# Kernel optimization log

Measured on AMD Instinct MI355X. Metric: run time of the kernel, lower is better.

## Reference

```python
import jax, jax.numpy as jnp
import numpy as np

B, LN, LT, D, DIN, H = 8, 64, 256, 1024, 2048, 4
LN_EPS = 1e-5
F16_EPS = float(np.finfo(np.float16).eps)


def setup_inputs() -> dict:
    key = jax.random.key(0)
    ks = jax.random.split(key, 16)
    n = lambda k, sh: jax.random.normal(k, sh, dtype=jnp.float32)
    s = 0.02
    z = lambda sh: jnp.zeros(sh, jnp.float32)
    return {
        "text_embeds": n(ks[0], (B, LT, D)),
        "node_embeds": n(ks[1], (B, LN, D)),
        "Wq": n(ks[2], (D, H * D)) * s, "bq": z((H * D,)),
        "Wk": n(ks[3], (D, H * D)) * s, "bk": z((H * D,)),
        "Wv": n(ks[4], (D, H * D)) * s, "bv": z((H * D,)),
        "Wo": n(ks[5], (H * D, D)) * s, "bo": z((D,)),
        "ln_g": jnp.ones((D,), jnp.float32), "ln_b": z((D,)),
        "aqW": n(ks[6], (D, D)) * s, "aqb": z((D,)),
        "akW": n(ks[7], (D, D)) * s, "akb": z((D,)),
        "att_v": n(ks[8], (D,)) * (1.0 / np.sqrt(D)),
        "att_b": z((D,)),
        "dp1W": n(ks[9], (D, DIN // 2)) * s, "dp1b": z((DIN // 2,)),
        "dp2W": n(ks[10], (DIN // 2, DIN)) * s, "dp2b": z((DIN,)),
        "gnn_mask": jax.random.randint(ks[11], (B, LN), 0, 2),
        "lm_mask": jax.random.randint(ks[12], (B, LT), 0, 2),
    }


def _forward(text_embeds, node_embeds, Wq, bq, Wk, bk, Wv, bv, Wo, bo, ln_g, ln_b,
             aqW, aqb, akW, akb, att_v, att_b, dp1W, dp1b, dp2W, dp2b,
             gnn_mask, lm_mask):
    x = node_embeds  # (B, LN, D)

    # ---- selfAttention_prompt: each of 4 heads has full width D ----
    def heads(w, b):
        return (x @ w + b).reshape(B, LN, H, D).transpose(0, 2, 1, 3)  # (B,H,LN,D)

    Q, K, V = heads(Wq, bq), heads(Wk, bk), heads(Wv, bv)
    A = jnp.einsum('bhqd,bhkd->bhqk', Q, K) / jnp.sqrt(jnp.float32(D))
    A = jnp.where(gnn_mask[:, None, None, :] == 0, -jnp.inf, A)
    alpha = jax.nn.softmax(A, axis=-1)
    out = jnp.einsum('bhqk,bhkd->bhqd', alpha, V)
    out = out.transpose(0, 2, 1, 3).reshape(B, LN, H * D)
    out = out @ Wo + bo + x
    # LayerNorm (torch default eps=1e-5)
    mu = out.mean(-1, keepdims=True)
    var = ((out - mu) ** 2).mean(-1, keepdims=True)
    H2 = (out - mu) / jnp.sqrt(var + LN_EPS) * ln_g + ln_b  # (B, LN, D)

    # ---- AdditiveAttention (Bahdanau): value_proj is unused in the original ----
    q = H2 @ aqW + aqb            # (B, LN, D)
    k = text_embeds @ akW + akb   # (B, LT, D)
    e = jnp.einsum('bqkd,d->bqk',
                   jnp.tanh(q[:, :, None, :] + k[:, None, :, :] + att_b), att_v)
    e = jnp.where(lm_mask[:, None, :] == 0, -jnp.inf, e)
    w = jax.nn.softmax(e, axis=-1)            # (B, LN, LT)
    H3 = jnp.einsum('bqk,bkd->bqd', w, text_embeds)  # context with raw V

    # ---- filter_Pool: masked mean over nodes ----
    m = gnn_mask.astype(H3.dtype)[:, :, None]
    cnt = jnp.clip(m.sum(1), F16_EPS, None)   # (B, 1)
    H4 = (H3 * m).sum(1) / cnt                # (B, D)

    # ---- domain projector (exact GELU like torch) ----
    Z = jax.nn.gelu(H4 @ dp1W + dp1b, approximate=False) @ dp2W + dp2b
    return Z  # (B, DIN)


def reference(text_embeds, node_embeds, Wq, bq, Wk, bk, Wv, bv, Wo, bo, ln_g, ln_b,
              aqW, aqb, akW, akb, att_v, att_b, dp1W, dp1b, dp2W, dp2b,
              gnn_mask, lm_mask):
    return _forward(text_embeds, node_embeds, Wq, bq, Wk, bk, Wv, bv, Wo, bo,
                    ln_g, ln_b, aqW, aqb, akW, akb, att_v, att_b,
                    dp1W, dp1b, dp2W, dp2b, gnn_mask, lm_mask)
```

## Files before the change

### kernel.cpp

```cpp
#include <hip/hip_runtime.h>
#include <hip/hip_bf16.h>
#include <math.h>

#define NB 8
#define LNN 64
#define LTN 256
#define DD 1024
#define NH 4
#define HDD 4096
#define DINN 2048
#define DHN 1024

#define C_TANH 2.8853900817779268f

typedef __bf16 bf16x8 __attribute__((ext_vector_type(8)));
typedef float f32x4 __attribute__((ext_vector_type(4)));

__device__ __forceinline__ ushort f2b(float f) {
  unsigned int u = __builtin_bit_cast(unsigned int, f);
  u = (u + 0x7FFFu + ((u >> 16) & 1u)) >> 16;
  return (ushort)u;
}

__global__ __launch_bounds__(256) void prep(const float* __restrict__ node,
                                            ushort* __restrict__ node_bf,
                                            const float* __restrict__ text,
                                            ushort* __restrict__ text_bf,
                                            const float* __restrict__ Wq,
                                            const float* __restrict__ Wk,
                                            const float* __restrict__ Wv,
                                            const float* __restrict__ Wo,
                                            const float* __restrict__ aqW,
                                            const float* __restrict__ akW,
                                            ushort* __restrict__ TwtQKV,
                                            ushort* __restrict__ TwtWo,
                                            ushort* __restrict__ TwtAQ) {
  int bid = blockIdx.x;
  int t = threadIdx.x;
  if (bid < 1280) {
    const float* in;
    ushort* out;
    int i;
    if (bid < 256) { in = node; out = node_bf; i = (bid * 256 + t) * 8; }
    else { in = text; out = text_bf; i = ((bid - 256) * 256 + t) * 8; }
    float4 a = *(const float4*)(in + i);
    float4 b = *(const float4*)(in + i + 4);
    ushort4 o0 = {f2b(a.x), f2b(a.y), f2b(a.z), f2b(a.w)};
    ushort4 o1 = {f2b(b.x), f2b(b.y), f2b(b.z), f2b(b.w)};
    *(ushort4*)(out + i) = o0;
    *(ushort4*)(out + i + 4) = o1;
    return;
  }
  bid -= 1280;
  const float* W;
  ushort* dst0;
  int K, N, tt;
  if (bid < 3072) {
    int z = bid >> 10;
    tt = bid & 1023;
    W = (z == 0) ? Wq : ((z == 1) ? Wk : Wv);
    dst0 = TwtQKV + (size_t)z * DD * HDD;
    K = DD; N = HDD;
  } else if (bid < 4096) {
    tt = bid - 3072; W = Wo; dst0 = TwtWo; K = HDD; N = DD;
  } else if (bid < 4352) {
    tt = bid - 4096; W = aqW; dst0 = TwtAQ; K = DD; N = DD;
  } else {
    tt = bid - 4352; W = akW; dst0 = TwtAQ + (size_t)DD * DD; K = DD; N = DD;
  }
  int ntn = N >> 6;
  int n0 = (tt % ntn) << 6, k0 = (tt / ntn) << 6;
  __shared__ float tf[64][65];
  int r = t >> 2, c4 = (t & 3) * 16;
  const float* src = W + (size_t)(k0 + r) * N + n0 + c4;
  float4 v0 = *(const float4*)(src);
  float4 v1 = *(const float4*)(src + 4);
  float4 v2 = *(const float4*)(src + 8);
  float4 v3 = *(const float4*)(src + 12);
  *(float4*)&tf[r][c4] = v0;
  *(float4*)&tf[r][c4 + 4] = v1;
  *(float4*)&tf[r][c4 + 8] = v2;
  *(float4*)&tf[r][c4 + 12] = v3;
  __syncthreads();
  int nl = t >> 2, kc = (t & 3) * 16;
  ushort tmp[16];
#pragma unroll
  for (int j = 0; j < 16; ++j) tmp[j] = f2b(tf[kc + j][nl]);
  ushort* dst = dst0 + (size_t)(n0 + nl) * K + k0 + kc;
  *(uint4*)(dst) = *(uint4*)&tmp[0];
  *(uint4*)(dst + 8) = *(uint4*)&tmp[8];
}

__global__ __launch_bounds__(256) void gemm_qkv3(const ushort* __restrict__ A,
                                                 const ushort* __restrict__ BtB,
                                                 const float* __restrict__ b0,
                                                 const float* __restrict__ b1,
                                                 const float* __restrict__ b2,
                                                 ushort* __restrict__ o0,
                                                 ushort* __restrict__ o1,
                                                 ushort* __restrict__ o2,
                                                 int M, int N, int K) {
  int z = blockIdx.z;
  const ushort* Bt = BtB + (size_t)z * N * K;
  const float* bias = (z == 0) ? b0 : ((z == 1) ? b1 : b2);
  ushort* Cout = (z == 0) ? o0 : ((z == 1) ? o1 : o2);
  __shared__ ushort Als[64 * 64];
  __shared__ ushort Bls[128 * 64];
  int tid = threadIdx.x;
  int m0 = blockIdx.y << 6, n0 = blockIdx.x << 7;
  int srow = tid >> 3, su = tid & 7;
  int sx = (su ^ (srow & 7)) * 8;
  const ushort* ga = A + (size_t)(m0 + srow) * K + su * 8;
  const ushort* gb = Bt + (size_t)(n0 + srow) * K + su * 8;
  int wa0 = srow * 64 + sx, wa1 = (srow + 32) * 64 + sx;
  int wb2 = (srow + 64) * 64 + sx, wb3 = (srow + 96) * 64 + sx;
  const size_t rs32 = (size_t)32 * K;
  int lane = tid & 63, w = tid >> 6;
  int wm = w >> 1, wn = w & 1;
  int r = lane & 15, kg = lane >> 4;
  f32x4 acc[2][4] = {};
  uint4 pa0 = *(const uint4*)(ga);
  uint4 pa1 = *(const uint4*)(ga + rs32);
  uint4 pb0 = *(const uint4*)(gb);
  uint4 pb1 = *(const uint4*)(gb + rs32);
  uint4 pb2 = *(const uint4*)(gb + 2 * rs32);
  uint4 pb3 = *(const uint4*)(gb + 3 * rs32);
  for (int k0 = 0; k0 < K; k0 += 64) {
    __syncthreads();
    *(uint4*)&Als[wa0] = pa0; *(uint4*)&Als[wa1] = pa1;
    *(uint4*)&Bls[wa0] = pb0; *(uint4*)&Bls[wa1] = pb1;
    *(uint4*)&Bls[wb2] = pb2; *(uint4*)&Bls[wb3] = pb3;
    __syncthreads();
    int kn = k0 + 64;
    if (kn < K) {
      pa0 = *(const uint4*)(ga + kn);
      pa1 = *(const uint4*)(ga + rs32 + kn);
      pb0 = *(const uint4*)(gb + kn);
      pb1 = *(const uint4*)(gb + rs32 + kn);
      pb2 = *(const uint4*)(gb + 2 * rs32 + kn);
      pb3 = *(const uint4*)(gb + 3 * rs32 + kn);
    }
#pragma unroll
    for (int h = 0; h < 2; ++h) {
      int sa = ((h * 4 + kg) ^ (r & 7)) * 8;
      bf16x8 af[2], bfr[4];
#pragma unroll
      for (int m = 0; m < 2; ++m)
        af[m] = *(const bf16x8*)&Als[(wm * 32 + m * 16 + r) * 64 + sa];
#pragma unroll
      for (int n = 0; n < 4; ++n)
        bfr[n] = *(const bf16x8*)&Bls[(wn * 64 + n * 16 + r) * 64 + sa];
#pragma unroll
      for (int m = 0; m < 2; ++m)
#pragma unroll
        for (int n = 0; n < 4; ++n)
          acc[m][n] = __builtin_amdgcn_mfma_f32_16x16x32_bf16(af[m], bfr[n], acc[m][n], 0, 0, 0);
    }
  }
#pragma unroll
  for (int m = 0; m < 2; ++m)
#pragma unroll
    for (int n = 0; n < 4; ++n) {
      f32x4 a = acc[m][n];
#pragma unroll
      for (int v = 0; v < 4; ++v) {
        int row = m0 + wm * 32 + m * 16 + kg * 4 + v;
        int col = n0 + wn * 64 + n * 16 + r;
        Cout[(size_t)row * N + col] = f2b(a[v] + bias[col]);
      }
    }
}

__global__ __launch_bounds__(256) void gemm_wo_split(const ushort* __restrict__ A,
                                                     const ushort* __restrict__ Bt,
                                                     float* __restrict__ P,
                                                     int M, int N, int K) {
  __shared__ ushort Als[64 * 64];
  __shared__ ushort Bls[128 * 64];
  int tid = threadIdx.x;
  int m0 = blockIdx.y << 6, n0 = blockIdx.x << 7;
  int Ks = K >> 2, kbase = blockIdx.z * Ks;
  int srow = tid >> 3, su = tid & 7;
  int sx = (su ^ (srow & 7)) * 8;
  const ushort* ga = A + (size_t)(m0 + srow) * K + kbase + su * 8;
  const ushort* gb = Bt + (size_t)(n0 + srow) * K + kbase + su * 8;
  int wa0 = srow * 64 + sx, wa1 = (srow + 32) * 64 + sx;
  int wb2 = (srow + 64) * 64 + sx, wb3 = (srow + 96) * 64 + sx;
  const size_t rs32 = (size_t)32 * K;
  int lane = tid & 63, w = tid >> 6;
  int wm = w >> 1, wn = w & 1;
  int r = lane & 15, kg = lane >> 4;
  f32x4 acc[2][4] = {};
  uint4 pa0 = *(const uint4*)(ga);
  uint4 pa1 = *(const uint4*)(ga + rs32);
  uint4 pb0 = *(const uint4*)(gb);
  uint4 pb1 = *(const uint4*)(gb + rs32);
  uint4 pb2 = *(const uint4*)(gb + 2 * rs32);
  uint4 pb3 = *(const uint4*)(gb + 3 * rs32);
  for (int k0 = 0; k0 < Ks; k0 += 64) {
    __syncthreads();
    *(uint4*)&Als[wa0] = pa0; *(uint4*)&Als[wa1] = pa1;
    *(uint4*)&Bls[wa0] = pb0; *(uint4*)&Bls[wa1] = pb1;
    *(uint4*)&Bls[wb2] = pb2; *(uint4*)&Bls[wb3] = pb3;
    __syncthreads();
    int kn = k0 + 64;
    if (kn < Ks) {
      pa0 = *(const uint4*)(ga + kn);
      pa1 = *(const uint4*)(ga + rs32 + kn);
      pb0 = *(const uint4*)(gb + kn);
      pb1 = *(const uint4*)(gb + rs32 + kn);
      pb2 = *(const uint4*)(gb + 2 * rs32 + kn);
      pb3 = *(const uint4*)(gb + 3 * rs32 + kn);
    }
#pragma unroll
    for (int h = 0; h < 2; ++h) {
      int sa = ((h * 4 + kg) ^ (r & 7)) * 8;
      bf16x8 af[2], bfr[4];
#pragma unroll
      for (int m = 0; m < 2; ++m)
        af[m] = *(const bf16x8*)&Als[(wm * 32 + m * 16 + r) * 64 + sa];
#pragma unroll
      for (int n = 0; n < 4; ++n)
        bfr[n] = *(const bf16x8*)&Bls[(wn * 64 + n * 16 + r) * 64 + sa];
#pragma unroll
      for (int m = 0; m < 2; ++m)
#pragma unroll
        for (int n = 0; n < 4; ++n)
          acc[m][n] = __builtin_amdgcn_mfma_f32_16x16x32_bf16(af[m], bfr[n], acc[m][n], 0, 0, 0);
    }
  }
#pragma unroll
  for (int m = 0; m < 2; ++m)
#pragma unroll
    for (int n = 0; n < 4; ++n) {
      f32x4 a = acc[m][n];
#pragma unroll
      for (int v = 0; v < 4; ++v) {
        int row = m0 + wm * 32 + m * 16 + kg * 4 + v;
        int col = n0 + wn * 64 + n * 16 + r;
        P[((size_t)blockIdx.z * M + row) * N + col] = a[v];
      }
    }
}

__global__ __launch_bounds__(256) void gemm_aqak(const ushort* __restrict__ H2,
                                                 const ushort* __restrict__ Tbf,
                                                 const ushort* __restrict__ TwtAQ,
                                                 const float* __restrict__ aqb,
                                                 const float* __restrict__ akb,
                                                 const float* __restrict__ attb,
                                                 float* __restrict__ QBu,
                                                 float* __restrict__ KAB,
                                                 int N, int K) {
  __shared__ ushort Als[64 * 64];
  __shared__ ushort Bls[128 * 64];
  int tid = threadIdx.x;
  int gm0 = blockIdx.y << 6, n0 = blockIdx.x << 7;
  const ushort* Abase;
  const ushort* Bt;
  const float* bias;
  const float* bias2;
  float* Obase;
  if (gm0 < 512) {
    Abase = H2 + (size_t)gm0 * K;
    Bt = TwtAQ;
    bias = aqb; bias2 = nullptr;
    Obase = QBu + (size_t)gm0 * N;
  } else {
    Abase = Tbf + (size_t)(gm0 - 512) * K;
    Bt = TwtAQ + (size_t)N * K;
    bias = akb; bias2 = attb;
    Obase = KAB + (size_t)(gm0 - 512) * N;
  }
  int srow = tid >> 3, su = tid & 7;
  int sx = (su ^ (srow & 7)) * 8;
  const ushort* ga = Abase + (size_t)srow * K + su * 8;
  const ushort* gb = Bt + (size_t)(n0 + srow) * K + su * 8;
  int wa0 = srow * 64 + sx, wa1 = (srow + 32) * 64 + sx;
  int wb2 = (srow + 64) * 64 + sx, wb3 = (srow + 96) * 64 + sx;
  const size_t rs32 = (size_t)32 * K;
  int lane = tid & 63, w = tid >> 6;
  int wm = w >> 1, wn = w & 1;
  int r = lane & 15, kg = lane >> 4;
  f32x4 acc[2][4] = {};
  uint4 pa0 = *(const uint4*)(ga);
  uint4 pa1 = *(const uint4*)(ga + rs32);
  uint4 pb0 = *(const uint4*)(gb);
  uint4 pb1 = *(const uint4*)(gb + rs32);
  uint4 pb2 = *(const uint4*)(gb + 2 * rs32);
  uint4 pb3 = *(const uint4*)(gb + 3 * rs32);
  for (int k0 = 0; k0 < K; k0 += 64) {
    __syncthreads();
    *(uint4*)&Als[wa0] = pa0; *(uint4*)&Als[wa1] = pa1;
    *(uint4*)&Bls[wa0] = pb0; *(uint4*)&Bls[wa1] = pb1;
    *(uint4*)&Bls[wb2] = pb2; *(uint4*)&Bls[wb3] = pb3;
    __syncthreads();
    int kn = k0 + 64;
    if (kn < K) {
      pa0 = *(const uint4*)(ga + kn);
      pa1 = *(const uint4*)(ga + rs32 + kn);
      pb0 = *(const uint4*)(gb + kn);
      pb1 = *(const uint4*)(gb + rs32 + kn);
      pb2 = *(const uint4*)(gb + 2 * rs32 + kn);
      pb3 = *(const uint4*)(gb + 3 * rs32 + kn);
    }
#pragma unroll
    for (int h = 0; h < 2; ++h) {
      int sa = ((h * 4 + kg) ^ (r & 7)) * 8;
      bf16x8 af[2], bfr[4];
#pragma unroll
      for (int m = 0; m < 2; ++m)
        af[m] = *(const bf16x8*)&Als[(wm * 32 + m * 16 + r) * 64 + sa];
#pragma unroll
      for (int n = 0; n < 4; ++n)
        bfr[n] = *(const bf16x8*)&Bls[(wn * 64 + n * 16 + r) * 64 + sa];
#pragma unroll
      for (int m = 0; m < 2; ++m)
#pragma unroll
        for (int n = 0; n < 4; ++n)
          acc[m][n] = __builtin_amdgcn_mfma_f32_16x16x32_bf16(af[m], bfr[n], acc[m][n], 0, 0, 0);
    }
  }
#pragma unroll
  for (int m = 0; m < 2; ++m)
#pragma unroll
    for (int n = 0; n < 4; ++n) {
      f32x4 a = acc[m][n];
#pragma unroll
      for (int v = 0; v < 4; ++v) {
        int lrow = wm * 32 + m * 16 + kg * 4 + v;
        int col = n0 + wn * 64 + n * 16 + r;
        float x = a[v] + bias[col];
        if (bias2) x += bias2[col];
        Obase[(size_t)lrow * N + col] = x * C_TANH;
      }
    }
}

__global__ __launch_bounds__(256) void wo_ln(const float* __restrict__ P,
                                             const float* __restrict__ bo,
                                             const float* __restrict__ node,
                                             const float* __restrict__ g,
                                             const float* __restrict__ be,
                                             ushort* __restrict__ Y) {
  int row = blockIdx.x, tid = threadIdx.x;
  int c = tid * 4;
  const size_t MN = (size_t)512 * 1024;
  size_t o = (size_t)row * DD + c;
  float4 v0 = *(const float4*)(P + o);
  float4 v1 = *(const float4*)(P + MN + o);
  float4 v2 = *(const float4*)(P + 2 * MN + o);
  float4 v3 = *(const float4*)(P + 3 * MN + o);
  float4 rv = *(const float4*)(node + o);
  float4 bv = *(const float4*)(bo + c);
  float4 v;
  v.x = v0.x + v1.x + v2.x + v3.x + rv.x + bv.x;
  v.y = v0.y + v1.y + v2.y + v3.y + rv.y + bv.y;
  v.z = v0.z + v1.z + v2.z + v3.z + rv.z + bv.z;
  v.w = v0.w + v1.w + v2.w + v3.w + rv.w + bv.w;
  float s = v.x + v.y + v.z + v.w;
  float ss = v.x * v.x + v.y * v.y + v.z * v.z + v.w * v.w;
  for (int o2 = 32; o2; o2 >>= 1) {
    s += __shfl_xor(s, o2, 64);
    ss += __shfl_xor(ss, o2, 64);
  }
  __shared__ float rb_[8];
  int lane = tid & 63, w = tid >> 6;
  if (lane == 0) { rb_[w] = s; rb_[4 + w] = ss; }
  __syncthreads();
  s = rb_[0] + rb_[1] + rb_[2] + rb_[3];
  ss = rb_[4] + rb_[5] + rb_[6] + rb_[7];
  float mu = s * (1.f / 1024.f);
  float var = ss * (1.f / 1024.f) - mu * mu;
  float rstd = rsqrtf(var + 1e-5f);
  ushort4 o4;
  o4.x = f2b((v.x - mu) * rstd * g[c + 0] + be[c + 0]);
  o4.y = f2b((v.y - mu) * rstd * g[c + 1] + be[c + 1]);
  o4.z = f2b((v.z - mu) * rstd * g[c + 2] + be[c + 2]);
  o4.w = f2b((v.w - mu) * rstd * g[c + 3] + be[c + 3]);
  *(ushort4*)(Y + (size_t)row * DD + c) = o4;
}

__global__ __launch_bounds__(256) void attn_qk(const ushort* __restrict__ Qb,
                                               const ushort* __restrict__ Kb,
                                               float* __restrict__ Sp) {
  int bh = blockIdx.x, ks = blockIdx.y;
  int b = bh >> 2;
  size_t base = ((size_t)b * LNN) * HDD + (size_t)(bh & 3) * DD + ks * 128;
  __shared__ ushort Als[64 * 64];
  __shared__ ushort Bls[64 * 64];
  int tid = threadIdx.x;
  int srow = tid >> 2, su0 = (tid & 3) * 2;
  const ushort* ga = Qb + base + (size_t)srow * HDD + su0 * 8;
  const ushort* gb = Kb + base + (size_t)srow * HDD + su0 * 8;
  int wa0 = srow * 64 + ((su0) ^ (srow & 7)) * 8;
  int wa1 = srow * 64 + ((su0 + 1) ^ (srow & 7)) * 8;
  int lane = tid & 63, w = tid >> 6;
  int wm = w >> 1, wn = w & 1;
  int r = lane & 15, kg = lane >> 4;
  f32x4 acc[2][2] = {};
  uint4 pa0 = *(const uint4*)(ga);
  uint4 pa1 = *(const uint4*)(ga + 8);
  uint4 pb0 = *(const uint4*)(gb);
  uint4 pb1 = *(const uint4*)(gb + 8);
  for (int k0 = 0; k0 < 128; k0 += 64) {
    __syncthreads();
    *(uint4*)&Als[wa0] = pa0; *(uint4*)&Als[wa1] = pa1;
    *(uint4*)&Bls[wa0] = pb0; *(uint4*)&Bls[wa1] = pb1;
    __syncthreads();
    if (k0 == 0) {
      pa0 = *(const uint4*)(ga + 64);
      pa1 = *(const uint4*)(ga + 64 + 8);
      pb0 = *(const uint4*)(gb + 64);
      pb1 = *(const uint4*)(gb + 64 + 8);
    }
#pragma unroll
    for (int h = 0; h < 2; ++h) {
      int sa = ((h * 4 + kg) ^ (r & 7)) * 8;
      bf16x8 af[2], bfr[2];
#pragma unroll
      for (int m = 0; m < 2; ++m)
        af[m] = *(const bf16x8*)&Als[(wm * 32 + m * 16 + r) * 64 + sa];
#pragma unroll
      for (int n = 0; n < 2; ++n)
        bfr[n] = *(const bf16x8*)&Bls[(wn * 32 + n * 16 + r) * 64 + sa];
#pragma unroll
      for (int m = 0; m < 2; ++m)
#pragma unroll
        for (int n = 0; n < 2; ++n)
          acc[m][n] = __builtin_amdgcn_mfma_f32_16x16x32_bf16(af[m], bfr[n], acc[m][n], 0, 0, 0);
    }
  }
  float* out = Sp + ((size_t)ks * 32 + bh) * 4096;
#pragma unroll
  for (int m = 0; m < 2; ++m)
#pragma unroll
    for (int n = 0; n < 2; ++n) {
      f32x4 a = acc[m][n];
#pragma unroll
      for (int v = 0; v < 4; ++v) {
        int row = wm * 32 + m * 16 + kg * 4 + v;
        int col = wn * 32 + n * 16 + r;
        out[row * 64 + col] = a[v];
      }
    }
}

__global__ __launch_bounds__(256) void attn_pv(const float* __restrict__ Sp,
                                               const ushort* __restrict__ Vb,
                                               const int* __restrict__ gmask,
                                               ushort* __restrict__ AO) {
  int bid = blockIdx.x;
  int bh = bid >> 3, dt = bid & 7;
  int b = bh >> 2;
  int d0 = dt * 128;
  size_t base = ((size_t)b * LNN) * HDD + (size_t)(bh & 3) * DD;
  __shared__ float S[64][68];
  __shared__ ushort Pls[64 * 72];
  __shared__ ushort Vt[128 * 72];
  int tid = threadIdx.x;
  int lane = tid & 63, w = tid >> 6;
  {
    int fbase = tid * 16;
    float a[16];
#pragma unroll
    for (int i = 0; i < 16; i += 4) {
      float4 v = *(const float4*)(Sp + (size_t)bh * 4096 + fbase + i);
      a[i] = v.x; a[i + 1] = v.y; a[i + 2] = v.z; a[i + 3] = v.w;
    }
#pragma unroll
    for (int ks = 1; ks < 8; ++ks) {
      const float* p = Sp + ((size_t)ks * 32 + bh) * 4096 + fbase;
#pragma unroll
      for (int i = 0; i < 16; i += 4) {
        float4 v = *(const float4*)(p + i);
        a[i] += v.x; a[i + 1] += v.y; a[i + 2] += v.z; a[i + 3] += v.w;
      }
    }
    int q = fbase >> 6, k = fbase & 63;
#pragma unroll
    for (int i = 0; i < 16; ++i) S[q][k + i] = a[i];
  }
  {
    int kq = lane, dq = w * 32;
    const ushort* src = Vb + base + (size_t)kq * HDD + d0 + dq;
    uint4 v0 = *(const uint4*)src;
    uint4 v1 = *(const uint4*)(src + 8);
    uint4 v2 = *(const uint4*)(src + 16);
    uint4 v3 = *(const uint4*)(src + 24);
    ushort tmp[32];
    *(uint4*)&tmp[0] = v0; *(uint4*)&tmp[8] = v1;
    *(uint4*)&tmp[16] = v2; *(uint4*)&tmp[24] = v3;
#pragma unroll
    for (int j = 0; j < 32; ++j) Vt[(dq + j) * 72 + kq] = tmp[j];
  }
  __syncthreads();
  bool valid = gmask[b * LNN + lane] != 0;
  for (int i = 0; i < 16; ++i) {
    int q = w * 16 + i;
    float v = valid ? S[q][lane] * 0.03125f : -__builtin_inff();
    float mx = v;
    for (int o = 32; o; o >>= 1) mx = fmaxf(mx, __shfl_xor(mx, o, 64));
    float e = valid ? __expf(v - mx) : 0.f;
    float s = e;
    for (int o = 32; o; o >>= 1) s += __shfl_xor(s, o, 64);
    Pls[q * 72 + lane] = f2b(__fdividef(e, s));
  }
  __syncthreads();
  int wm = w >> 1, wn = w & 1;
  int r = lane & 15, kg = lane >> 4;
  f32x4 acc[2][4] = {};
#pragma unroll
  for (int h = 0; h < 2; ++h) {
    int ko = h * 32 + kg * 8;
    bf16x8 af[2], bfr[4];
#pragma unroll
    for (int m = 0; m < 2; ++m)
      af[m] = *(const bf16x8*)&Pls[(wm * 32 + m * 16 + r) * 72 + ko];
#pragma unroll
    for (int n = 0; n < 4; ++n)
      bfr[n] = *(const bf16x8*)&Vt[(wn * 64 + n * 16 + r) * 72 + ko];
#pragma unroll
    for (int m = 0; m < 2; ++m)
#pragma unroll
      for (int n = 0; n < 4; ++n)
        acc[m][n] = __builtin_amdgcn_mfma_f32_16x16x32_bf16(af[m], bfr[n], acc[m][n], 0, 0, 0);
  }
#pragma unroll
  for (int m = 0; m < 2; ++m)
#pragma unroll
    for (int n = 0; n < 4; ++n) {
      f32x4 a = acc[m][n];
#pragma unroll
      for (int v = 0; v < 4; ++v) {
        int q = wm * 32 + m * 16 + kg * 4 + v;
        int col = wn * 64 + n * 16 + r;
        AO[base + (size_t)q * HDD + d0 + col] = f2b(a[v]);
      }
    }
}

__global__ __launch_bounds__(256) void addatt_e(const float* __restrict__ QBu,
                                                const float* __restrict__ KAB,
                                                const float* __restrict__ av_,
                                                float* __restrict__ E8) {
  int ds = blockIdx.x, qt = blockIdx.y, b = blockIdx.z;
  int tid = threadIdx.x;
  __shared__ float qs[8][128];
  __shared__ float avs[128];
  __shared__ float red[4];
  int bq0 = b * LNN + qt * 8;
  {
    int qq = tid >> 5, dd = (tid & 31) * 4;
    *(float4*)&qs[qq][dd] = *(const float4*)(QBu + (size_t)(bq0 + qq) * DD + ds * 128 + dd);
  }
  float av = (tid < 128) ? av_[ds * 128 + tid] : 0.f;
  if (tid < 128) avs[tid] = av;
  float s = av;
  for (int o = 32; o; o >>= 1) s += __shfl_xor(s, o, 64);
  int lane = tid & 63, w = tid >> 6;
  if (lane == 0) red[w] = s;
  __syncthreads();
  float sumav = red[0] + red[1] + red[2] + red[3];
  const float* kr = KAB + (size_t)(b * LTN + tid) * DD + ds * 128;
  float ac[8] = {};
#pragma unroll 2
  for (int d = 0; d < 128; d += 4) {
    float4 kv = *(const float4*)(kr + d);
    float4 av4 = *(const float4*)&avs[d];
#pragma unroll
    for (int qq = 0; qq < 8; ++qq) {
      float4 q4 = *(const float4*)&qs[qq][d];
      ac[qq] = fmaf(av4.x, __builtin_amdgcn_rcpf(__builtin_amdgcn_exp2f(q4.x + kv.x) + 1.f), ac[qq]);
      ac[qq] = fmaf(av4.y, __builtin_amdgcn_rcpf(__builtin_amdgcn_exp2f(q4.y + kv.y) + 1.f), ac[qq]);
      ac[qq] = fmaf(av4.z, __builtin_amdgcn_rcpf(__builtin_amdgcn_exp2f(q4.z + kv.z) + 1.f), ac[qq]);
      ac[qq] = fmaf(av4.w, __builtin_amdgcn_rcpf(__builtin_amdgcn_exp2f(q4.w + kv.w) + 1.f), ac[qq]);
    }
  }
  size_t ebase = ((size_t)ds * 512 + bq0) * LTN + tid;
#pragma unroll
  for (int qq = 0; qq < 8; ++qq)
    E8[ebase + (size_t)qq * LTN] = sumav - 2.f * ac[qq];
}

__global__ __launch_bounds__(256) void addatt_sm(const float* __restrict__ E8,
                                                 const int* __restrict__ lmask,
                                                 float* __restrict__ Wv) {
  int bq = blockIdx.x;
  int b = bq >> 6;
  int tid = threadIdx.x;
  __shared__ float rb_[8];
  float e = 0.f;
#pragma unroll
  for (int ks = 0; ks < 8; ++ks)
    e += E8[((size_t)ks * 512 + bq) * LTN + tid];
  bool valid = lmask[b * LTN + tid] != 0;
  float v = valid ? e : -__builtin_inff();
  int lane = tid & 63, w = tid >> 6;
  float m = v;
  for (int o = 32; o; o >>= 1) m = fmaxf(m, __shfl_xor(m, o, 64));
  if (lane == 0) rb_[w] = m;
  __syncthreads();
  m = fmaxf(fmaxf(rb_[0], rb_[1]), fmaxf(rb_[2], rb_[3]));
  float ex = valid ? __expf(v - m) : 0.f;
  float sm = ex;
  for (int o = 32; o; o >>= 1) sm += __shfl_xor(sm, o, 64);
  if (lane == 0) rb_[4 + w] = sm;
  __syncthreads();
  sm = rb_[4] + rb_[5] + rb_[6] + rb_[7];
  Wv[(size_t)bq * LTN + tid] = __fdividef(ex, sm);
}

__global__ __launch_bounds__(256) void addatt_pool(const float* __restrict__ Wv,
                                                   const float* __restrict__ text,
                                                   const int* __restrict__ gmask,
                                                   float* __restrict__ H4) {
  int dt = blockIdx.x, b = blockIdx.y;
  int tid = threadIdx.x;
  __shared__ float cf[LTN];
  float c = 0.f, cnt = 0.f;
#pragma unroll 8
  for (int q = 0; q < LNN; ++q) {
    float m = (gmask[b * LNN + q] != 0) ? 1.f : 0.f;
    cnt += m;
    c = fmaf(m, Wv[(size_t)(b * LNN + q) * LTN + tid], c);
  }
  cf[tid] = c;
  cnt = fmaxf(cnt, 9.765625e-04f);
  __syncthreads();
  int d = dt * 256 + tid;
  const float* tb = text + (size_t)b * LTN * DD + d;
  float acc = 0.f;
#pragma unroll 8
  for (int k = 0; k < LTN; ++k) acc = fmaf(cf[k], tb[(size_t)k * DD], acc);
  H4[b * DD + d] = acc / cnt;
}

__global__ __launch_bounds__(256) void dp_split(const float* __restrict__ X,
                                                const float* __restrict__ W,
                                                float* __restrict__ P,
                                                int K, int N) {
  int jt = blockIdx.x, kt = blockIdx.y;
  int t = threadIdx.x;
  __shared__ float xs[8][32];
  if (t < 64) {
    int b = t >> 3, kk = (t & 7) * 4;
    *(float4*)&xs[b][kk] = *(const float4*)(X + (size_t)b * K + kt * 32 + kk);
  }
  __syncthreads();
  int j = jt * 64 + (t & 63);
  int bg = (t >> 6) * 2;
  const float* wp = W + (size_t)(kt * 32) * N + j;
  float a0 = 0.f, a1 = 0.f;
#pragma unroll
  for (int k = 0; k < 32; ++k) {
    float w = wp[(size_t)k * N];
    a0 = fmaf(xs[bg + 0][k], w, a0);
    a1 = fmaf(xs[bg + 1][k], w, a1);
  }
  P[((size_t)kt * 8 + bg + 0) * N + j] = a0;
  P[((size_t)kt * 8 + bg + 1) * N + j] = a1;
}

template <int GELU>
__global__ __launch_bounds__(256) void dp_reduce(const float* __restrict__ P,
                                                 const float* __restrict__ bias,
                                                 float* __restrict__ O, int N) {
  int b = blockIdx.y;
  int j = blockIdx.x * 256 + threadIdx.x;
  float s = bias[j];
#pragma unroll 8
  for (int kt = 0; kt < 32; ++kt) s += P[((size_t)kt * 8 + b) * N + j];
  if constexpr (GELU) s = 0.5f * s * (1.f + erff(s * 0.70710678118654752440f));
  O[(size_t)b * N + j] = s;
}

extern "C" void kernel_launch(void* const* d_in, const int* in_sizes, int n_in,
                              void* d_out, int out_size, void* d_ws, size_t ws_size,
                              hipStream_t stream) {
  const float* text = (const float*)d_in[0];
  const float* node = (const float*)d_in[1];
  const float* Wq = (const float*)d_in[2];
  const float* bq = (const float*)d_in[3];
  const float* Wk = (const float*)d_in[4];
  const float* bk = (const float*)d_in[5];
  const float* Wv = (const float*)d_in[6];
  const float* bv = (const float*)d_in[7];
  const float* Wo = (const float*)d_in[8];
  const float* bo = (const float*)d_in[9];
  const float* lng = (const float*)d_in[10];
  const float* lnb = (const float*)d_in[11];
  const float* aqW = (const float*)d_in[12];
  const float* aqb = (const float*)d_in[13];
  const float* akW = (const float*)d_in[14];
  const float* akb = (const float*)d_in[15];
  const float* attv = (const float*)d_in[16];
  const float* attb = (const float*)d_in[17];
  const float* dp1W = (const float*)d_in[18];
  const float* dp1b = (const float*)d_in[19];
  const float* dp2W = (const float*)d_in[20];
  const float* dp2b = (const float*)d_in[21];
  const int* gmask = (const int*)d_in[22];
  const int* lmask = (const int*)d_in[23];
  (void)in_sizes; (void)n_in; (void)out_size; (void)ws_size;

  char* base = (char*)d_ws;
#define MB(x) (((size_t)(x)) << 20)
  ushort* TwtQKV = (ushort*)(base);
  ushort* TwtWo = (ushort*)(base + MB(24));
  ushort* TwtAQ = (ushort*)(base + MB(32));
  ushort* node_bf = (ushort*)(base + MB(36));
  ushort* text_bf = (ushort*)(base + MB(37));
  ushort* Qb = (ushort*)(base + MB(41));
  ushort* Kb = (ushort*)(base + MB(45));
  ushort* Vb = (ushort*)(base + MB(49));
  ushort* AO = (ushort*)(base + MB(53));
  float* Sp = (float*)(base + MB(57));
  float* P_Wo = (float*)(base + MB(61));
  ushort* H2 = (ushort*)(base + MB(69));
  float* QBu = (float*)(base + MB(70));
  float* KAB = (float*)(base + MB(72));
  float* E8 = (float*)(base + MB(80));
  float* Wvb = (float*)(base + MB(84));
  float* H4 = (float*)(base + MB(84) + (512 << 10));
  float* G = (float*)(base + MB(84) + (512 << 10) + 32768);
  float* P1 = (float*)(base + MB(85));
  float* P2 = (float*)(base + MB(86));
  float* Z = (float*)d_out;
#undef MB

  const int M1 = NB * LNN;
  dim3 blk(256);

  prep<<<dim3(5888), blk, 0, stream>>>(node, node_bf, text, text_bf,
                                       Wq, Wk, Wv, Wo, aqW, akW,
                                       TwtQKV, TwtWo, TwtAQ);

  gemm_qkv3<<<dim3(HDD / 128, M1 / 64, 3), blk, 0, stream>>>(node_bf, TwtQKV, bq, bk, bv, Qb, Kb, Vb, M1, HDD, DD);

  attn_qk<<<dim3(NB * NH, 8), blk, 0, stream>>>(Qb, Kb, Sp);
  attn_pv<<<dim3(NB * NH * 8), blk, 0, stream>>>(Sp, Vb, gmask, AO);

  gemm_wo_split<<<dim3(DD / 128, M1 / 64, 4), blk, 0, stream>>>(AO, TwtWo, P_Wo, M1, DD, HDD);
  wo_ln<<<dim3(M1), blk, 0, stream>>>(P_Wo, bo, node, lng, lnb, H2);

  gemm_aqak<<<dim3(DD / 128, 40), blk, 0, stream>>>(H2, text_bf, TwtAQ, aqb, akb, attb, QBu, KAB, DD, DD);

  addatt_e<<<dim3(8, 8, NB), blk, 0, stream>>>(QBu, KAB, attv, E8);
  addatt_sm<<<dim3(M1), blk, 0, stream>>>(E8, lmask, Wvb);
  addatt_pool<<<dim3(4, NB), blk, 0, stream>>>(Wvb, text, gmask, H4);

  dp_split<<<dim3(DHN / 64, 32), blk, 0, stream>>>(H4, dp1W, P1, DD, DHN);
  dp_reduce<1><<<dim3(DHN / 256, NB), blk, 0, stream>>>(P1, dp1b, G, DHN);
  dp_split<<<dim3(DINN / 64, 32), blk, 0, stream>>>(G, dp2W, P2, DHN, DINN);
  dp_reduce<0><<<dim3(DINN / 256, NB), blk, 0, stream>>>(P2, dp2b, Z, DINN);
}
```

Before: 162.0 us.

## Use 128x128 GEMM tiles, deepen Wo split-K, fuse GELU reduce into dp2

The three bf16 MFMA GEMMs (QKV, Wo, aq/ak) move from 64x128 to 128x128 tiles, so each warp computes a 64x64 sub-tile (4x4 MFMA accumulators) and more data is reused from LDS per global load. The Wo GEMM split-K factor goes from 4 to 8 to keep enough blocks, and wo_ln now sums 8 partial buffers. The dp1 reduce plus GELU is fused into the dp2 split kernel, dropping one launch and the G buffer round trip, though each block redoes its slice of the reduction. The bigger tiles halve the block count for the QKV and aqak GEMMs and raise register and LDS use per block, which may cut occupancy.

```diff
diff --git a/kernel.cpp b/kernel.cpp
--- a/kernel.cpp
+++ b/kernel.cpp
@@ -91,171 +91,160 @@
   *(uint4*)(dst + 8) = *(uint4*)&tmp[8];
 }
 
-__global__ __launch_bounds__(256) void gemm_qkv3(const ushort* __restrict__ A,
-                                                 const ushort* __restrict__ BtB,
-                                                 const float* __restrict__ b0,
-                                                 const float* __restrict__ b1,
-                                                 const float* __restrict__ b2,
-                                                 ushort* __restrict__ o0,
-                                                 ushort* __restrict__ o1,
-                                                 ushort* __restrict__ o2,
-                                                 int M, int N, int K) {
+
+__global__ __launch_bounds__(256) void gemm128_qkv3(const ushort* __restrict__ A,
+                                                    const ushort* __restrict__ BtB,
+                                                    const float* __restrict__ b0,
+                                                    const float* __restrict__ b1,
+                                                    const float* __restrict__ b2,
+                                                    ushort* __restrict__ o0,
+                                                    ushort* __restrict__ o1,
+                                                    ushort* __restrict__ o2,
+                                                    int M, int N, int K) {
   int z = blockIdx.z;
   const ushort* Bt = BtB + (size_t)z * N * K;
   const float* bias = (z == 0) ? b0 : ((z == 1) ? b1 : b2);
   ushort* Cout = (z == 0) ? o0 : ((z == 1) ? o1 : o2);
-  __shared__ ushort Als[64 * 64];
+  __shared__ ushort Als[128 * 64];
   __shared__ ushort Bls[128 * 64];
   int tid = threadIdx.x;
-  int m0 = blockIdx.y << 6, n0 = blockIdx.x << 7;
-  int srow = tid >> 3, su = tid & 7;
-  int sx = (su ^ (srow & 7)) * 8;
-  const ushort* ga = A + (size_t)(m0 + srow) * K + su * 8;
-  const ushort* gb = Bt + (size_t)(n0 + srow) * K + su * 8;
-  int wa0 = srow * 64 + sx, wa1 = (srow + 32) * 64 + sx;
-  int wb2 = (srow + 64) * 64 + sx, wb3 = (srow + 96) * 64 + sx;
-  const size_t rs32 = (size_t)32 * K;
+  int m0 = blockIdx.y << 7, n0 = blockIdx.x << 7;
+  int srow = tid >> 1, su0 = (tid & 1) * 4;
+  const ushort* ga = A + (size_t)(m0 + srow) * K + su0 * 8;
+  const ushort* gb = Bt + (size_t)(n0 + srow) * K + su0 * 8;
+  int wof[4];
+#pragma unroll
+  for (int j = 0; j < 4; ++j) wof[j] = srow * 64 + ((su0 + j) ^ (srow & 7)) * 8;
   int lane = tid & 63, w = tid >> 6;
   int wm = w >> 1, wn = w & 1;
   int r = lane & 15, kg = lane >> 4;
-  f32x4 acc[2][4] = {};
-  uint4 pa0 = *(const uint4*)(ga);
-  uint4 pa1 = *(const uint4*)(ga + rs32);
-  uint4 pb0 = *(const uint4*)(gb);
-  uint4 pb1 = *(const uint4*)(gb + rs32);
-  uint4 pb2 = *(const uint4*)(gb + 2 * rs32);
-  uint4 pb3 = *(const uint4*)(gb + 3 * rs32);
+  f32x4 acc[4][4] = {};
+  uint4 pa[4], pb[4];
+#pragma unroll
+  for (int j = 0; j < 4; ++j) { pa[j] = *(const uint4*)(ga + j * 8); pb[j] = *(const uint4*)(gb + j * 8); }
   for (int k0 = 0; k0 < K; k0 += 64) {
     __syncthreads();
-    *(uint4*)&Als[wa0] = pa0; *(uint4*)&Als[wa1] = pa1;
-    *(uint4*)&Bls[wa0] = pb0; *(uint4*)&Bls[wa1] = pb1;
-    *(uint4*)&Bls[wb2] = pb2; *(uint4*)&Bls[wb3] = pb3;
+#pragma unroll
+    for (int j = 0; j < 4; ++j) { *(uint4*)&Als[wof[j]] = pa[j]; *(uint4*)&Bls[wof[j]] = pb[j]; }
     __syncthreads();
     int kn = k0 + 64;
     if (kn < K) {
-      pa0 = *(const uint4*)(ga + kn);
-      pa1 = *(const uint4*)(ga + rs32 + kn);
-      pb0 = *(const uint4*)(gb + kn);
-      pb1 = *(const uint4*)(gb + rs32 + kn);
-      pb2 = *(const uint4*)(gb + 2 * rs32 + kn);
-      pb3 = *(const uint4*)(gb + 3 * rs32 + kn);
+#pragma unroll
+      for (int j = 0; j < 4; ++j) {
+        pa[j] = *(const uint4*)(ga + kn + j * 8);
+        pb[j] = *(const uint4*)(gb + kn + j * 8);
+      }
     }
 #pragma unroll
     for (int h = 0; h < 2; ++h) {
       int sa = ((h * 4 + kg) ^ (r & 7)) * 8;
-      bf16x8 af[2], bfr[4];
-#pragma unroll
-      for (int m = 0; m < 2; ++m)
-        af[m] = *(const bf16x8*)&Als[(wm * 32 + m * 16 + r) * 64 + sa];
+      bf16x8 af[4], bfr[4];
+#pragma unroll
+      for (int m = 0; m < 4; ++m)
+        af[m] = *(const bf16x8*)&Als[(wm * 64 + m * 16 + r) * 64 + sa];
 #pragma unroll
       for (int n = 0; n < 4; ++n)
         bfr[n] = *(const bf16x8*)&Bls[(wn * 64 + n * 16 + r) * 64 + sa];
 #pragma unroll
-      for (int m = 0; m < 2; ++m)
+      for (int m = 0; m < 4; ++m)
 #pragma unroll
         for (int n = 0; n < 4; ++n)
           acc[m][n] = __builtin_amdgcn_mfma_f32_16x16x32_bf16(af[m], bfr[n], acc[m][n], 0, 0, 0);
     }
   }
 #pragma unroll
-  for (int m = 0; m < 2; ++m)
+  for (int m = 0; m < 4; ++m)
 #pragma unroll
     for (int n = 0; n < 4; ++n) {
       f32x4 a = acc[m][n];
 #pragma unroll
       for (int v = 0; v < 4; ++v) {
-        int row = m0 + wm * 32 + m * 16 + kg * 4 + v;
+        int row = m0 + wm * 64 + m * 16 + kg * 4 + v;
         int col = n0 + wn * 64 + n * 16 + r;
         Cout[(size_t)row * N + col] = f2b(a[v] + bias[col]);
       }
     }
 }
 
-__global__ __launch_bounds__(256) void gemm_wo_split(const ushort* __restrict__ A,
-                                                     const ushort* __restrict__ Bt,
-                                                     float* __restrict__ P,
-                                                     int M, int N, int K) {
-  __shared__ ushort Als[64 * 64];
+__global__ __launch_bounds__(256) void gemm128_wo(const ushort* __restrict__ A,
+                                                  const ushort* __restrict__ Bt,
+                                                  float* __restrict__ P,
+                                                  int M, int N, int K) {
+  __shared__ ushort Als[128 * 64];
   __shared__ ushort Bls[128 * 64];
   int tid = threadIdx.x;
-  int m0 = blockIdx.y << 6, n0 = blockIdx.x << 7;
-  int Ks = K >> 2, kbase = blockIdx.z * Ks;
-  int srow = tid >> 3, su = tid & 7;
-  int sx = (su ^ (srow & 7)) * 8;
-  const ushort* ga = A + (size_t)(m0 + srow) * K + kbase + su * 8;
-  const ushort* gb = Bt + (size_t)(n0 + srow) * K + kbase + su * 8;
-  int wa0 = srow * 64 + sx, wa1 = (srow + 32) * 64 + sx;
-  int wb2 = (srow + 64) * 64 + sx, wb3 = (srow + 96) * 64 + sx;
-  const size_t rs32 = (size_t)32 * K;
+  int m0 = blockIdx.y << 7, n0 = blockIdx.x << 7;
+  int Ks = K >> 3, kbase = blockIdx.z * Ks;
+  int srow = tid >> 1, su0 = (tid & 1) * 4;
+  const ushort* ga = A + (size_t)(m0 + srow) * K + kbase + su0 * 8;
+  const ushort* gb = Bt + (size_t)(n0 + srow) * K + kbase + su0 * 8;
+  int wof[4];
+#pragma unroll
+  for (int j = 0; j < 4; ++j) wof[j] = srow * 64 + ((su0 + j) ^ (srow & 7)) * 8;
   int lane = tid & 63, w = tid >> 6;
   int wm = w >> 1, wn = w & 1;
   int r = lane & 15, kg = lane >> 4;
-  f32x4 acc[2][4] = {};
-  uint4 pa0 = *(const uint4*)(ga);
-  uint4 pa1 = *(const uint4*)(ga + rs32);
-  uint4 pb0 = *(const uint4*)(gb);
-  uint4 pb1 = *(const uint4*)(gb + rs32);
-  uint4 pb2 = *(const uint4*)(gb + 2 * rs32);
-  uint4 pb3 = *(const uint4*)(gb + 3 * rs32);
+  f32x4 acc[4][4] = {};
+  uint4 pa[4], pb[4];
+#pragma unroll
+  for (int j = 0; j < 4; ++j) { pa[j] = *(const uint4*)(ga + j * 8); pb[j] = *(const uint4*)(gb + j * 8); }
   for (int k0 = 0; k0 < Ks; k0 += 64) {
     __syncthreads();
-    *(uint4*)&Als[wa0] = pa0; *(uint4*)&Als[wa1] = pa1;
-    *(uint4*)&Bls[wa0] = pb0; *(uint4*)&Bls[wa1] = pb1;
-    *(uint4*)&Bls[wb2] = pb2; *(uint4*)&Bls[wb3] = pb3;
+#pragma unroll
+    for (int j = 0; j < 4; ++j) { *(uint4*)&Als[wof[j]] = pa[j]; *(uint4*)&Bls[wof[j]] = pb[j]; }
     __syncthreads();
     int kn = k0 + 64;
     if (kn < Ks) {
-      pa0 = *(const uint4*)(ga + kn);
-      pa1 = *(const uint4*)(ga + rs32 + kn);
-      pb0 = *(const uint4*)(gb + kn);
-      pb1 = *(const uint4*)(gb + rs32 + kn);
-      pb2 = *(const uint4*)(gb + 2 * rs32 + kn);
-      pb3 = *(const uint4*)(gb + 3 * rs32 + kn);
+#pragma unroll
+      for (int j = 0; j < 4; ++j) {
+        pa[j] = *(const uint4*)(ga + kn + j * 8);
+        pb[j] = *(const uint4*)(gb + kn + j * 8);
+      }
     }
 #pragma unroll
     for (int h = 0; h < 2; ++h) {
       int sa = ((h * 4 + kg) ^ (r & 7)) * 8;
-      bf16x8 af[2], bfr[4];
-#pragma unroll
-      for (int m = 0; m < 2; ++m)
-        af[m] = *(const bf16x8*)&Als[(wm * 32 + m * 16 + r) * 64 + sa];
+      bf16x8 af[4], bfr[4];
+#pragma unroll
+      for (int m = 0; m < 4; ++m)
+        af[m] = *(const bf16x8*)&Als[(wm * 64 + m * 16 + r) * 64 + sa];
 #pragma unroll
       for (int n = 0; n < 4; ++n)
         bfr[n] = *(const bf16x8*)&Bls[(wn * 64 + n * 16 + r) * 64 + sa];
 #pragma unroll
-      for (int m = 0; m < 2; ++m)
+      for (int m = 0; m < 4; ++m)
 #pragma unroll
         for (int n = 0; n < 4; ++n)
           acc[m][n] = __builtin_amdgcn_mfma_f32_16x16x32_bf16(af[m], bfr[n], acc[m][n], 0, 0, 0);
     }
   }
 #pragma unroll
-  for (int m = 0; m < 2; ++m)
+  for (int m = 0; m < 4; ++m)
 #pragma unroll
     for (int n = 0; n < 4; ++n) {
       f32x4 a = acc[m][n];
 #pragma unroll
       for (int v = 0; v < 4; ++v) {
-        int row = m0 + wm * 32 + m * 16 + kg * 4 + v;
+        int row = m0 + wm * 64 + m * 16 + kg * 4 + v;
         int col = n0 + wn * 64 + n * 16 + r;
         P[((size_t)blockIdx.z * M + row) * N + col] = a[v];
       }
     }
 }
 
-__global__ __launch_bounds__(256) void gemm_aqak(const ushort* __restrict__ H2,
-                                                 const ushort* __restrict__ Tbf,
-                                                 const ushort* __restrict__ TwtAQ,
-                                                 const float* __restrict__ aqb,
-                                                 const float* __restrict__ akb,
-                                                 const float* __restrict__ attb,
-                                                 float* __restrict__ QBu,
-                                                 float* __restrict__ KAB,
-                                                 int N, int K) {
-  __shared__ ushort Als[64 * 64];
+__global__ __launch_bounds__(256) void gemm128_aqak(const ushort* __restrict__ H2,
+                                                    const ushort* __restrict__ Tbf,
+                                                    const ushort* __restrict__ TwtAQ,
+                                                    const float* __restrict__ aqb,
+                                                    const float* __restrict__ akb,
+                                                    const float* __restrict__ attb,
+                                                    float* __restrict__ QBu,
+                                                    float* __restrict__ KAB,
+                                                    int N, int K) {
+  __shared__ ushort Als[128 * 64];
   __shared__ ushort Bls[128 * 64];
   int tid = threadIdx.x;
-  int gm0 = blockIdx.y << 6, n0 = blockIdx.x << 7;
+  int gm0 = blockIdx.y << 7, n0 = blockIdx.x << 7;
   const ushort* Abase;
   const ushort* Bt;
   const float* bias;
@@ -272,63 +261,57 @@
     bias = akb; bias2 = attb;
     Obase = KAB + (size_t)(gm0 - 512) * N;
   }
-  int srow = tid >> 3, su = tid & 7;
-  int sx = (su ^ (srow & 7)) * 8;
-  const ushort* ga = Abase + (size_t)srow * K + su * 8;
-  const ushort* gb = Bt + (size_t)(n0 + srow) * K + su * 8;
-  int wa0 = srow * 64 + sx, wa1 = (srow + 32) * 64 + sx;
-  int wb2 = (srow + 64) * 64 + sx, wb3 = (srow + 96) * 64 + sx;
-  const size_t rs32 = (size_t)32 * K;
+  int srow = tid >> 1, su0 = (tid & 1) * 4;
+  const ushort* ga = Abase + (size_t)srow * K + su0 * 8;
+  const ushort* gb = Bt + (size_t)(n0 + srow) * K + su0 * 8;
+  int wof[4];
+#pragma unroll
+  for (int j = 0; j < 4; ++j) wof[j] = srow * 64 + ((su0 + j) ^ (srow & 7)) * 8;
   int lane = tid & 63, w = tid >> 6;
   int wm = w >> 1, wn = w & 1;
   int r = lane & 15, kg = lane >> 4;
-  f32x4 acc[2][4] = {};
-  uint4 pa0 = *(const uint4*)(ga);
-  uint4 pa1 = *(const uint4*)(ga + rs32);
-  uint4 pb0 = *(const uint4*)(gb);
-  uint4 pb1 = *(const uint4*)(gb + rs32);
-  uint4 pb2 = *(const uint4*)(gb + 2 * rs32);
-  uint4 pb3 = *(const uint4*)(gb + 3 * rs32);
+  f32x4 acc[4][4] = {};
+  uint4 pa[4], pb[4];
+#pragma unroll
+  for (int j = 0; j < 4; ++j) { pa[j] = *(const uint4*)(ga + j * 8); pb[j] = *(const uint4*)(gb + j * 8); }
   for (int k0 = 0; k0 < K; k0 += 64) {
     __syncthreads();
-    *(uint4*)&Als[wa0] = pa0; *(uint4*)&Als[wa1] = pa1;
-    *(uint4*)&Bls[wa0] = pb0; *(uint4*)&Bls[wa1] = pb1;
-    *(uint4*)&Bls[wb2] = pb2; *(uint4*)&Bls[wb3] = pb3;
+#pragma unroll
+    for (int j = 0; j < 4; ++j) { *(uint4*)&Als[wof[j]] = pa[j]; *(uint4*)&Bls[wof[j]] = pb[j]; }
     __syncthreads();
     int kn = k0 + 64;
     if (kn < K) {
-      pa0 = *(const uint4*)(ga + kn);
-      pa1 = *(const uint4*)(ga + rs32 + kn);
-      pb0 = *(const uint4*)(gb + kn);
-      pb1 = *(const uint4*)(gb + rs32 + kn);
-      pb2 = *(const uint4*)(gb + 2 * rs32 + kn);
-      pb3 = *(const uint4*)(gb + 3 * rs32 + kn);
+#pragma unroll
+      for (int j = 0; j < 4; ++j) {
+        pa[j] = *(const uint4*)(ga + kn + j * 8);
+        pb[j] = *(const uint4*)(gb + kn + j * 8);
+      }
     }
 #pragma unroll
     for (int h = 0; h < 2; ++h) {
       int sa = ((h * 4 + kg) ^ (r & 7)) * 8;
-      bf16x8 af[2], bfr[4];
-#pragma unroll
-      for (int m = 0; m < 2; ++m)
-        af[m] = *(const bf16x8*)&Als[(wm * 32 + m * 16 + r) * 64 + sa];
+      bf16x8 af[4], bfr[4];
+#pragma unroll
+      for (int m = 0; m < 4; ++m)
+        af[m] = *(const bf16x8*)&Als[(wm * 64 + m * 16 + r) * 64 + sa];
 #pragma unroll
       for (int n = 0; n < 4; ++n)
         bfr[n] = *(const bf16x8*)&Bls[(wn * 64 + n * 16 + r) * 64 + sa];
 #pragma unroll
-      for (int m = 0; m < 2; ++m)
+      for (int m = 0; m < 4; ++m)
 #pragma unroll
         for (int n = 0; n < 4; ++n)
           acc[m][n] = __builtin_amdgcn_mfma_f32_16x16x32_bf16(af[m], bfr[n], acc[m][n], 0, 0, 0);
     }
   }
 #pragma unroll
-  for (int m = 0; m < 2; ++m)
+  for (int m = 0; m < 4; ++m)
 #pragma unroll
     for (int n = 0; n < 4; ++n) {
       f32x4 a = acc[m][n];
 #pragma unroll
       for (int v = 0; v < 4; ++v) {
-        int lrow = wm * 32 + m * 16 + kg * 4 + v;
+        int lrow = wm * 64 + m * 16 + kg * 4 + v;
         int col = n0 + wn * 64 + n * 16 + r;
         float x = a[v] + bias[col];
         if (bias2) x += bias2[col];
@@ -347,17 +330,15 @@
   int c = tid * 4;
   const size_t MN = (size_t)512 * 1024;
   size_t o = (size_t)row * DD + c;
-  float4 v0 = *(const float4*)(P + o);
-  float4 v1 = *(const float4*)(P + MN + o);
-  float4 v2 = *(const float4*)(P + 2 * MN + o);
-  float4 v3 = *(const float4*)(P + 3 * MN + o);
   float4 rv = *(const float4*)(node + o);
   float4 bv = *(const float4*)(bo + c);
   float4 v;
-  v.x = v0.x + v1.x + v2.x + v3.x + rv.x + bv.x;
-  v.y = v0.y + v1.y + v2.y + v3.y + rv.y + bv.y;
-  v.z = v0.z + v1.z + v2.z + v3.z + rv.z + bv.z;
-  v.w = v0.w + v1.w + v2.w + v3.w + rv.w + bv.w;
+  v.x = rv.x + bv.x; v.y = rv.y + bv.y; v.z = rv.z + bv.z; v.w = rv.w + bv.w;
+#pragma unroll
+  for (int s8 = 0; s8 < 8; ++s8) {
+    float4 p = *(const float4*)(P + s8 * MN + o);
+    v.x += p.x; v.y += p.y; v.z += p.z; v.w += p.w;
+  }
   float s = v.x + v.y + v.z + v.w;
   float ss = v.x * v.x + v.y * v.y + v.z * v.z + v.w * v.w;
   for (int o2 = 32; o2; o2 >>= 1) {
@@ -662,6 +643,37 @@
   P[((size_t)kt * 8 + bg + 1) * N + j] = a1;
 }
 
+__global__ __launch_bounds__(256) void dp_split2g(const float* __restrict__ P1,
+                                                  const float* __restrict__ b1,
+                                                  const float* __restrict__ W,
+                                                  float* __restrict__ P,
+                                                  int K, int N) {
+  int jt = blockIdx.x, kt = blockIdx.y;
+  int t = threadIdx.x;
+  __shared__ float xs[8][32];
+  {
+    int b = t >> 5, kk = t & 31;
+    int j = kt * 32 + kk;
+    float s = b1[j];
+#pragma unroll 8
+    for (int p = 0; p < 32; ++p) s += P1[((size_t)p * 8 + b) * K + j];
+    xs[b][kk] = 0.5f * s * (1.f + erff(s * 0.70710678118654752440f));
+  }
+  __syncthreads();
+  int j = jt * 64 + (t & 63);
+  int bg = (t >> 6) * 2;
+  const float* wp = W + (size_t)(kt * 32) * N + j;
+  float a0 = 0.f, a1 = 0.f;
+#pragma unroll
+  for (int k = 0; k < 32; ++k) {
+    float w = wp[(size_t)k * N];
+    a0 = fmaf(xs[bg + 0][k], w, a0);
+    a1 = fmaf(xs[bg + 1][k], w, a1);
+  }
+  P[((size_t)kt * 8 + bg + 0) * N + j] = a0;
+  P[((size_t)kt * 8 + bg + 1) * N + j] = a1;
+}
+
 template <int GELU>
 __global__ __launch_bounds__(256) void dp_reduce(const float* __restrict__ P,
                                                  const float* __restrict__ bias,
@@ -717,15 +729,14 @@
   ushort* AO = (ushort*)(base + MB(53));
   float* Sp = (float*)(base + MB(57));
   float* P_Wo = (float*)(base + MB(61));
-  ushort* H2 = (ushort*)(base + MB(69));
-  float* QBu = (float*)(base + MB(70));
-  float* KAB = (float*)(base + MB(72));
-  float* E8 = (float*)(base + MB(80));
-  float* Wvb = (float*)(base + MB(84));
-  float* H4 = (float*)(base + MB(84) + (512 << 10));
-  float* G = (float*)(base + MB(84) + (512 << 10) + 32768);
-  float* P1 = (float*)(base + MB(85));
-  float* P2 = (float*)(base + MB(86));
+  ushort* H2 = (ushort*)(base + MB(77));
+  float* QBu = (float*)(base + MB(78));
+  float* KAB = (float*)(base + MB(80));
+  float* E8 = (float*)(base + MB(88));
+  float* Wvb = (float*)(base + MB(92));
+  float* H4 = (float*)(base + MB(92) + (512 << 10));
+  float* P1 = (float*)(base + MB(93));
+  float* P2 = (float*)(base + MB(94));
   float* Z = (float*)d_out;
 #undef MB
 
@@ -736,22 +747,21 @@
                                        Wq, Wk, Wv, Wo, aqW, akW,
                                        TwtQKV, TwtWo, TwtAQ);
 
-  gemm_qkv3<<<dim3(HDD / 128, M1 / 64, 3), blk, 0, stream>>>(node_bf, TwtQKV, bq, bk, bv, Qb, Kb, Vb, M1, HDD, DD);
+  gemm128_qkv3<<<dim3(HDD / 128, M1 / 128, 3), blk, 0, stream>>>(node_bf, TwtQKV, bq, bk, bv, Qb, Kb, Vb, M1, HDD, DD);
 
   attn_qk<<<dim3(NB * NH, 8), blk, 0, stream>>>(Qb, Kb, Sp);
   attn_pv<<<dim3(NB * NH * 8), blk, 0, stream>>>(Sp, Vb, gmask, AO);
 
-  gemm_wo_split<<<dim3(DD / 128, M1 / 64, 4), blk, 0, stream>>>(AO, TwtWo, P_Wo, M1, DD, HDD);
+  gemm128_wo<<<dim3(DD / 128, M1 / 128, 8), blk, 0, stream>>>(AO, TwtWo, P_Wo, M1, DD, HDD);
   wo_ln<<<dim3(M1), blk, 0, stream>>>(P_Wo, bo, node, lng, lnb, H2);
 
-  gemm_aqak<<<dim3(DD / 128, 40), blk, 0, stream>>>(H2, text_bf, TwtAQ, aqb, akb, attb, QBu, KAB, DD, DD);
+  gemm128_aqak<<<dim3(DD / 128, 20), blk, 0, stream>>>(H2, text_bf, TwtAQ, aqb, akb, attb, QBu, KAB, DD, DD);
 
   addatt_e<<<dim3(8, 8, NB), blk, 0, stream>>>(QBu, KAB, attv, E8);
   addatt_sm<<<dim3(M1), blk, 0, stream>>>(E8, lmask, Wvb);
   addatt_pool<<<dim3(4, NB), blk, 0, stream>>>(Wvb, text, gmask, H4);
 
   dp_split<<<dim3(DHN / 64, 32), blk, 0, stream>>>(H4, dp1W, P1, DD, DHN);
-  dp_reduce<1><<<dim3(DHN / 256, NB), blk, 0, stream>>>(P1, dp1b, G, DHN);
-  dp_split<<<dim3(DINN / 64, 32), blk, 0, stream>>>(G, dp2W, P2, DHN, DINN);
+  dp_split2g<<<dim3(DINN / 64, 32), blk, 0, stream>>>(P1, dp1b, dp2W, P2, DHN, DINN);
   dp_reduce<0><<<dim3(DINN / 256, NB), blk, 0, stream>>>(P2, dp2b, Z, DINN);
 }
```

Result: slower. 269.2 us (+66.2%).
